# Kernel tuning notes

Measured on AMD Instinct MI355X. Metric: run time of the kernel, lower is better.

## Reference

```python
import jax, jax.numpy as jnp
import numpy as np

L, B, S, D = 12, 4, 1024, 1024
EPS = 1e-5  # torch LayerNorm default


def setup_inputs() -> dict:
    key = jax.random.key(0)
    k1, k2, k3 = jax.random.split(key, 3)
    return {
        "layer_history": jax.random.normal(k1, (L, B, S, D), jnp.float32),
        "current": jax.random.normal(k2, (B, S, D), jnp.float32),
        "w": jax.random.normal(k3, (D,), jnp.float32) * (1.0 / D ** 0.5),
        "gamma": jnp.ones((D,), jnp.float32),
        "beta": jnp.zeros((D,), jnp.float32),
    }


def reference(layer_history, current, w, gamma, beta):
    # V: [L+1, B, S, D] -- all history layers plus the current layer
    V = jnp.concatenate([layer_history, current[None]], axis=0)
    L1 = V.shape[0]
    Bc, Sc, Dc = current.shape

    # LayerNorm over last dim (biased variance, like torch)
    mu = jnp.mean(V, axis=-1, keepdims=True)
    var = jnp.mean((V - mu) ** 2, axis=-1, keepdims=True)
    K = (V - mu) * jax.lax.rsqrt(var + EPS) * gamma + beta

    # pseudo-query scores: one scalar per (layer, batch, key-pos)
    scores = jnp.einsum('d,lbsd->bls', w, K)  # [B, L1, S]

    # broadcast over query index t, causal mask on key index s (s > t masked)
    causal = jnp.triu(jnp.ones((Sc, Sc), bool), 1)          # [t, s]
    s4 = jnp.where(causal[None, :, None, :], -jnp.inf,
                   scores[:, None, :, :])                   # [B, S, L1, S]

    # softmax jointly over all (layer, key-pos) pairs
    wts = jax.nn.softmax(s4.reshape(Bc, Sc, L1 * Sc), axis=-1)
    wts = wts.reshape(Bc, Sc, L1, Sc)

    # weighted sum over values (V un-normalized)
    h = jnp.einsum('btls,lbsd->btd', wts, V)  # [B, S, D]
    return h
```

## Files before the change

### kernel.cpp

```cpp
#include <hip/hip_runtime.h>
#include <math.h>

namespace {
constexpr int L1 = 13;
constexpr int LH = 12;
constexpr int B  = 4;
constexpr int S  = 1024;
constexpr int D  = 1024;
constexpr int NCH  = 32;
constexpr int CH   = S / NCH;
constexpr int DBLK = D / 256;
constexpr int RPB  = 8;
constexpr int NPS  = B * S / RPB;

constexpr int OFF_Z    = 0;
constexpr int OFF_ZCUM = B * S;
constexpr int OFF_CS   = 2 * B * S;
constexpr int OFF_PS   = OFF_CS + B * NCH * D;
constexpr float EPS = 1e-5f;

typedef float float4n __attribute__((ext_vector_type(4)));
}

__global__ __launch_bounds__(256) void arm_k1(const float* __restrict__ hist,
                                              const float* __restrict__ cur,
                                              const float* __restrict__ w,
                                              const float* __restrict__ gamma,
                                              const float* __restrict__ beta,
                                              float* __restrict__ U,
                                              float* __restrict__ ws) {
    const int tid = threadIdx.x, lane = tid & 63, wid = tid >> 6;
    const int blk = blockIdx.x;
    const int row0 = blk * RPB + wid * 2;
    const int d0 = lane * 4;

    __shared__ float cs[4][D];

    float4n wg[4];
    float swg_p = 0.f, swb_p = 0.f;
#pragma unroll
    for (int j = 0; j < 4; j++) {
        int d = d0 + j * 256;
        float4n wv = *(const float4n*)(w + d);
        float4n gv = *(const float4n*)(gamma + d);
        float4n bv = *(const float4n*)(beta + d);
        wg[j] = wv * gv;
        swg_p += wg[j].x + wg[j].y + wg[j].z + wg[j].w;
        float4n wb = wv * bv;
        swb_p += wb.x + wb.y + wb.z + wb.w;
    }
#pragma unroll
    for (int o = 32; o > 0; o >>= 1) {
        swg_p += __shfl_xor(swg_p, o);
        swb_p += __shfl_xor(swb_p, o);
    }
    const float swg = swg_p, swb = swb_p;

#pragma unroll
    for (int r = 0; r < 2; r++) {
        const size_t rowoff = (size_t)(row0 + r) * D;
        float4n acc[4] = {{0,0,0,0},{0,0,0,0},{0,0,0,0},{0,0,0,0}};
        float z = 0.f;

#pragma unroll 2
        for (int l = 0; l < L1; l++) {
            const float* row = (l < LH ? hist + (size_t)l * (B * S * D) : cur) + rowoff;
            float4n v[4];
#pragma unroll
            for (int j = 0; j < 4; j++) v[j] = *(const float4n*)(row + d0 + j * 256);

            float s1 = 0.f, s2 = 0.f, sw = 0.f;
#pragma unroll
            for (int j = 0; j < 4; j++) {
                s1 += v[j].x + v[j].y + v[j].z + v[j].w;
                s2 += v[j].x * v[j].x + v[j].y * v[j].y + v[j].z * v[j].z + v[j].w * v[j].w;
                sw += wg[j].x * v[j].x + wg[j].y * v[j].y + wg[j].z * v[j].z + wg[j].w * v[j].w;
            }
#pragma unroll
            for (int o = 32; o > 0; o >>= 1) {
                s1 += __shfl_xor(s1, o);
                s2 += __shfl_xor(s2, o);
                sw += __shfl_xor(sw, o);
            }
            float mu   = s1 * (1.0f / D);
            float var  = s2 * (1.0f / D) - mu * mu;
            float rstd = rsqrtf(var + EPS);
            float p = __expf(rstd * (sw - mu * swg) + swb);
#pragma unroll
            for (int j = 0; j < 4; j++) acc[j] += v[j] * p;
            z += p;
        }

#pragma unroll
        for (int j = 0; j < 4; j++)
            *(float4n*)(U + rowoff + d0 + j * 256) = acc[j];
        if (lane == 0) ws[OFF_Z + row0 + r] = z;

        if (r == 0) {
#pragma unroll
            for (int j = 0; j < 4; j++)
                *(float4n*)&cs[wid][d0 + j * 256] = acc[j];
        } else {
#pragma unroll
            for (int j = 0; j < 4; j++) {
                float4n t = *(float4n*)&cs[wid][d0 + j * 256];
                *(float4n*)&cs[wid][d0 + j * 256] = t + acc[j];
            }
        }
    }

    __syncthreads();
    const int c = tid * 4;
    float4n ps = *(float4n*)&cs[0][c];
    ps += *(float4n*)&cs[1][c];
    ps += *(float4n*)&cs[2][c];
    ps += *(float4n*)&cs[3][c];
    *(float4n*)(ws + OFF_PS + (size_t)blk * D + c) = ps;
}

__global__ void arm_k2(float* __restrict__ ws) {
    int blk = blockIdx.x;
    int tid = threadIdx.x;
    if (blk >= B * NCH) {
        int b = blk - B * NCH;
        const float* z = ws + OFF_Z + b * S;
        float* zc = ws + OFF_ZCUM + b * S;
        float v[4];
        float loc = 0.f;
#pragma unroll
        for (int j = 0; j < 4; j++) { v[j] = z[tid * 4 + j]; loc += v[j]; }
        __shared__ float lds[256];
        lds[tid] = loc; __syncthreads();
        for (int off = 1; off < 256; off <<= 1) {
            float t = (tid >= off) ? lds[tid - off] : 0.f;
            __syncthreads();
            lds[tid] += t;
            __syncthreads();
        }
        float run = lds[tid] - loc;
#pragma unroll
        for (int j = 0; j < 4; j++) { run += v[j]; zc[tid * 4 + j] = run; }
        return;
    }
    int b = blk / NCH, ch = blk % NCH;
    int c = tid * 4;
    float4n s = {0, 0, 0, 0};
#pragma unroll
    for (int k = 0; k < 4; k++)
        s += *(const float4n*)(ws + OFF_PS + (size_t)((b * S / RPB) + ch * 4 + k) * D + c);
    *(float4n*)(ws + OFF_CS + (size_t)blk * D + c) = s;
}

__global__ void arm_k3(float* __restrict__ U, const float* __restrict__ ws) {
    int blk = blockIdx.x;
    int dblk = blk % DBLK;
    int rem = blk / DBLK;
    int ch = rem % NCH, b = rem / NCH;
    int d = dblk * 256 + threadIdx.x;

    const float* cs = ws + OFF_CS + b * NCH * D + d;
    float run = 0.f;
    for (int c2 = 0; c2 < ch; c2++) run += cs[(size_t)c2 * D];

    const float* zc = ws + OFF_ZCUM + b * S + ch * CH;
    float* Ub = U + ((size_t)b * S + ch * CH) * D + d;
#pragma unroll
    for (int j = 0; j < CH; j++) {
        run += Ub[(size_t)j * D];
        Ub[(size_t)j * D] = run / zc[j];
    }
}

extern "C" void kernel_launch(void* const* d_in, const int* in_sizes, int n_in,
                              void* d_out, int out_size, void* d_ws, size_t ws_size,
                              hipStream_t stream) {
    const float* hist  = (const float*)d_in[0];
    const float* cur   = (const float*)d_in[1];
    const float* w     = (const float*)d_in[2];
    const float* gamma = (const float*)d_in[3];
    const float* beta  = (const float*)d_in[4];
    float* out = (float*)d_out;
    float* ws  = (float*)d_ws;

    arm_k1<<<B * S / RPB, 256, 0, stream>>>(hist, cur, w, gamma, beta, out, ws);
    arm_k2<<<B * NCH + B, 256, 0, stream>>>(ws);
    arm_k3<<<B * NCH * DBLK, 256, 0, stream>>>(out, ws);
}
```

Measured before the change: 60.59 us.

## Merge scan and finalize kernels, one row per wave in history pass

The z-cumsum and chunk-sum kernel is folded into the final normalization kernel. Each block now redoes the z prefix scan for its batch and sums the per-block partial sums directly from the workspace. The first kernel drops to one row per wave with four rows per block, which doubles the block count. This removes one launch and its inter-kernel dependency. In exchange it adds redundant scans and longer serial partial-sum loops, up to 248 strided loads per thread for late chunks.

```diff
diff --git a/kernel.cpp b/kernel.cpp
--- a/kernel.cpp
+++ b/kernel.cpp
@@ -10,13 +10,12 @@
 constexpr int NCH  = 32;
 constexpr int CH   = S / NCH;
 constexpr int DBLK = D / 256;
-constexpr int RPB  = 8;
+constexpr int RPB  = 4;
 constexpr int NPS  = B * S / RPB;
+constexpr int PSPC = CH / RPB;
 
-constexpr int OFF_Z    = 0;
-constexpr int OFF_ZCUM = B * S;
-constexpr int OFF_CS   = 2 * B * S;
-constexpr int OFF_PS   = OFF_CS + B * NCH * D;
+constexpr int OFF_Z  = 0;
+constexpr int OFF_PS = B * S;
 constexpr float EPS = 1e-5f;
 
 typedef float float4n __attribute__((ext_vector_type(4)));
@@ -31,8 +30,9 @@
                                               float* __restrict__ ws) {
     const int tid = threadIdx.x, lane = tid & 63, wid = tid >> 6;
     const int blk = blockIdx.x;
-    const int row0 = blk * RPB + wid * 2;
+    const int row = blk * RPB + wid;
     const int d0 = lane * 4;
+    const size_t rowoff = (size_t)row * D;
 
     __shared__ float cs[4][D];
 
@@ -56,58 +56,44 @@
     }
     const float swg = swg_p, swb = swb_p;
 
-#pragma unroll
-    for (int r = 0; r < 2; r++) {
-        const size_t rowoff = (size_t)(row0 + r) * D;
-        float4n acc[4] = {{0,0,0,0},{0,0,0,0},{0,0,0,0},{0,0,0,0}};
-        float z = 0.f;
+    float4n acc[4] = {{0,0,0,0},{0,0,0,0},{0,0,0,0},{0,0,0,0}};
+    float z = 0.f;
 
 #pragma unroll 2
-        for (int l = 0; l < L1; l++) {
-            const float* row = (l < LH ? hist + (size_t)l * (B * S * D) : cur) + rowoff;
-            float4n v[4];
+    for (int l = 0; l < L1; l++) {
+        const float* vrow = (l < LH ? hist + (size_t)l * (B * S * D) : cur) + rowoff;
+        float4n v[4];
 #pragma unroll
-            for (int j = 0; j < 4; j++) v[j] = *(const float4n*)(row + d0 + j * 256);
+        for (int j = 0; j < 4; j++) v[j] = *(const float4n*)(vrow + d0 + j * 256);
 
-            float s1 = 0.f, s2 = 0.f, sw = 0.f;
+        float s1 = 0.f, s2 = 0.f, sw = 0.f;
 #pragma unroll
-            for (int j = 0; j < 4; j++) {
-                s1 += v[j].x + v[j].y + v[j].z + v[j].w;
-                s2 += v[j].x * v[j].x + v[j].y * v[j].y + v[j].z * v[j].z + v[j].w * v[j].w;
-                sw += wg[j].x * v[j].x + wg[j].y * v[j].y + wg[j].z * v[j].z + wg[j].w * v[j].w;
-            }
+        for (int j = 0; j < 4; j++) {
+            s1 += v[j].x + v[j].y + v[j].z + v[j].w;
+            s2 += v[j].x * v[j].x + v[j].y * v[j].y + v[j].z * v[j].z + v[j].w * v[j].w;
+            sw += wg[j].x * v[j].x + wg[j].y * v[j].y + wg[j].z * v[j].z + wg[j].w * v[j].w;
+        }
 #pragma unroll
-            for (int o = 32; o > 0; o >>= 1) {
-                s1 += __shfl_xor(s1, o);
-                s2 += __shfl_xor(s2, o);
-                sw += __shfl_xor(sw, o);
-            }
-            float mu   = s1 * (1.0f / D);
-            float var  = s2 * (1.0f / D) - mu * mu;
-            float rstd = rsqrtf(var + EPS);
-            float p = __expf(rstd * (sw - mu * swg) + swb);
+        for (int o = 32; o > 0; o >>= 1) {
+            s1 += __shfl_xor(s1, o);
+            s2 += __shfl_xor(s2, o);
+            sw += __shfl_xor(sw, o);
+        }
+        float mu   = s1 * (1.0f / D);
+        float var  = s2 * (1.0f / D) - mu * mu;
+        float rstd = rsqrtf(var + EPS);
+        float p = __expf(rstd * (sw - mu * swg) + swb);
 #pragma unroll
-            for (int j = 0; j < 4; j++) acc[j] += v[j] * p;
-            z += p;
-        }
+        for (int j = 0; j < 4; j++) acc[j] += v[j] * p;
+        z += p;
+    }
 
 #pragma unroll
-        for (int j = 0; j < 4; j++)
-            *(float4n*)(U + rowoff + d0 + j * 256) = acc[j];
-        if (lane == 0) ws[OFF_Z + row0 + r] = z;
-
-        if (r == 0) {
-#pragma unroll
-            for (int j = 0; j < 4; j++)
-                *(float4n*)&cs[wid][d0 + j * 256] = acc[j];
-        } else {
-#pragma unroll
-            for (int j = 0; j < 4; j++) {
-                float4n t = *(float4n*)&cs[wid][d0 + j * 256];
-                *(float4n*)&cs[wid][d0 + j * 256] = t + acc[j];
-            }
-        }
+    for (int j = 0; j < 4; j++) {
+        *(float4n*)(U + rowoff + d0 + j * 256) = acc[j];
+        *(float4n*)&cs[wid][d0 + j * 256] = acc[j];
     }
+    if (lane == 0) ws[OFF_Z + row] = z;
 
     __syncthreads();
     const int c = tid * 4;
@@ -118,56 +104,47 @@
     *(float4n*)(ws + OFF_PS + (size_t)blk * D + c) = ps;
 }
 
-__global__ void arm_k2(float* __restrict__ ws) {
-    int blk = blockIdx.x;
-    int tid = threadIdx.x;
-    if (blk >= B * NCH) {
-        int b = blk - B * NCH;
-        const float* z = ws + OFF_Z + b * S;
-        float* zc = ws + OFF_ZCUM + b * S;
-        float v[4];
-        float loc = 0.f;
+__global__ __launch_bounds__(256) void arm_k2(float* __restrict__ U,
+                                              const float* __restrict__ ws) {
+    const int blk = blockIdx.x;
+    const int dblk = blk % DBLK;
+    const int rem = blk / DBLK;
+    const int ch = rem % NCH, b = rem / NCH;
+    const int tid = threadIdx.x;
+
+    const float* z = ws + OFF_Z + b * S;
+    float v[4];
+    float loc = 0.f;
 #pragma unroll
-        for (int j = 0; j < 4; j++) { v[j] = z[tid * 4 + j]; loc += v[j]; }
-        __shared__ float lds[256];
-        lds[tid] = loc; __syncthreads();
-        for (int off = 1; off < 256; off <<= 1) {
-            float t = (tid >= off) ? lds[tid - off] : 0.f;
-            __syncthreads();
-            lds[tid] += t;
-            __syncthreads();
-        }
-        float run = lds[tid] - loc;
+    for (int j = 0; j < 4; j++) { v[j] = z[tid * 4 + j]; loc += v[j]; }
+    __shared__ float lds[256];
+    __shared__ float zcl[CH];
+    lds[tid] = loc; __syncthreads();
+    for (int off = 1; off < 256; off <<= 1) {
+        float t = (tid >= off) ? lds[tid - off] : 0.f;
+        __syncthreads();
+        lds[tid] += t;
+        __syncthreads();
+    }
+    float zrun = lds[tid] - loc;
 #pragma unroll
-        for (int j = 0; j < 4; j++) { run += v[j]; zc[tid * 4 + j] = run; }
-        return;
+    for (int j = 0; j < 4; j++) {
+        zrun += v[j];
+        int r = tid * 4 + j;
+        if (r >= ch * CH && r < ch * CH + CH) zcl[r - ch * CH] = zrun;
     }
-    int b = blk / NCH, ch = blk % NCH;
-    int c = tid * 4;
-    float4n s = {0, 0, 0, 0};
-#pragma unroll
-    for (int k = 0; k < 4; k++)
-        s += *(const float4n*)(ws + OFF_PS + (size_t)((b * S / RPB) + ch * 4 + k) * D + c);
-    *(float4n*)(ws + OFF_CS + (size_t)blk * D + c) = s;
-}
+    __syncthreads();
 
-__global__ void arm_k3(float* __restrict__ U, const float* __restrict__ ws) {
-    int blk = blockIdx.x;
-    int dblk = blk % DBLK;
-    int rem = blk / DBLK;
-    int ch = rem % NCH, b = rem / NCH;
-    int d = dblk * 256 + threadIdx.x;
+    const int d = dblk * 256 + tid;
+    const float* ps = ws + OFF_PS + (size_t)(b * (S / RPB)) * D + d;
+    float run = 0.f;
+    for (int r = 0; r < ch * PSPC; r++) run += ps[(size_t)r * D];
 
-    const float* cs = ws + OFF_CS + b * NCH * D + d;
-    float run = 0.f;
-    for (int c2 = 0; c2 < ch; c2++) run += cs[(size_t)c2 * D];
-
-    const float* zc = ws + OFF_ZCUM + b * S + ch * CH;
     float* Ub = U + ((size_t)b * S + ch * CH) * D + d;
 #pragma unroll
     for (int j = 0; j < CH; j++) {
         run += Ub[(size_t)j * D];
-        Ub[(size_t)j * D] = run / zc[j];
+        Ub[(size_t)j * D] = run / zcl[j];
     }
 }
 
@@ -183,6 +160,5 @@
     float* ws  = (float*)d_ws;
 
     arm_k1<<<B * S / RPB, 256, 0, stream>>>(hist, cur, w, gamma, beta, out, ws);
-    arm_k2<<<B * NCH + B, 256, 0, stream>>>(ws);
-    arm_k3<<<B * NCH * DBLK, 256, 0, stream>>>(out, ws);
+    arm_k2<<<B * NCH * DBLK, 256, 0, stream>>>(out, ws);
 }
```

Result: slower. 130.9 us (+116.1%).
